# Kernel optimization log

Hardware: AMD Instinct MI355X
Metric: run time of the kernel (lower is better)

## Reference

```python
import jax, jax.numpy as jnp
import numpy as np

N_NODES = 50000
N_EDGES = 600000
D = 128
R = 8


def setup_inputs() -> dict:
    key = jax.random.key(0)
    ks = jax.random.split(key, 10)
    return {
        "node_ids": jnp.arange(N_NODES, dtype=jnp.int32),
        "src": jax.random.randint(ks[0], (N_EDGES,), 0, N_NODES, dtype=jnp.int32),
        "dst": jax.random.randint(ks[1], (N_EDGES,), 0, N_NODES, dtype=jnp.int32),
        "etype": jax.random.randint(ks[2], (N_EDGES,), 0, R, dtype=jnp.int32),
        "emb": jax.random.normal(ks[3], (N_NODES, D), dtype=jnp.float32) * 0.02,
        "W1": jax.random.normal(ks[4], (R, D, D), dtype=jnp.float32) * 0.05,
        "Wself1": jax.random.normal(ks[5], (D, D), dtype=jnp.float32) * 0.05,
        "b1": jnp.zeros((D,), dtype=jnp.float32),
        "W2": jax.random.normal(ks[6], (R, D, D), dtype=jnp.float32) * 0.05,
        "Wself2": jax.random.normal(ks[7], (D, D), dtype=jnp.float32) * 0.05,
        "b2": jnp.zeros((D,), dtype=jnp.float32),
    }


def rgcn_layer(h, W, Wself, b, src, dst, etype, n_nodes):
    # relation-wise transform of all node features: [R, N, d_out]
    hr = jnp.einsum('nd,rdo->rno', h, W)
    # per-edge gather of (relation, src) -> message, then scatter-sum to dst
    msgs = hr[etype, src]                                   # [E, d_out]
    agg = jax.ops.segment_sum(msgs, dst, num_segments=n_nodes)
    # self-loop + bias (activation=None, feat_drop=0)
    return agg + h @ Wself + b


def reference(node_ids, src, dst, etype, emb, W1, Wself1, b1, W2, Wself2, b2):
    h0 = emb[node_ids]                                      # embedding lookup over all nodes
    h1 = rgcn_layer(h0, W1, Wself1, b1, src, dst, etype, emb.shape[0])
    h2 = rgcn_layer(h1, W2, Wself2, b2, src, dst, etype, emb.shape[0])
    return h2
```

## Files before the change

kernel.cpp:

```cpp
#include <hip/hip_runtime.h>
#include <hip/hip_bf16.h>

#define NN 50000
#define NE 600000
#define DD 128
#define NR 8
#define NCHUNK ((NN + 255) / 256)

typedef __attribute__((ext_vector_type(8))) short bf16x8;
typedef __attribute__((ext_vector_type(4))) float f32x4;

__device__ __forceinline__ unsigned short f2bf(float f) {
  __hip_bfloat16 h = __float2bfloat16(f);
  return *reinterpret_cast<unsigned short*>(&h);
}
__device__ __forceinline__ unsigned pk2(float lo, float hi) {
  return (unsigned)f2bf(lo) | ((unsigned)f2bf(hi) << 16);
}
__device__ __forceinline__ float bflo(unsigned u) { return __uint_as_float(u << 16); }
__device__ __forceinline__ float bfhi(unsigned u) { return __uint_as_float(u & 0xffff0000u); }

__global__ __launch_bounds__(128) void convw_kernel(
    const float* __restrict__ W1, const float* __restrict__ Ws1,
    const float* __restrict__ W2, const float* __restrict__ Ws2,
    unsigned short* __restrict__ WT)
{
  const int m = blockIdx.y, o = blockIdx.x, d = threadIdx.x;
  const float* src;
  if (m < 8)       src = W1 + (size_t)m * DD * DD;
  else if (m == 8) src = Ws1;
  else if (m < 17) src = W2 + (size_t)(m - 9) * DD * DD;
  else             src = Ws2;
  WT[(size_t)m * DD * DD + o * DD + d] = f2bf(src[(size_t)d * DD + o]);
}

template<int AF32, int OUTF32>
__global__ __launch_bounds__(256) void transform_mfma(
    const void* __restrict__ hin, const int* __restrict__ ids,
    const unsigned short* __restrict__ WT,
    const float* __restrict__ bias,
    unsigned short* __restrict__ hr,
    void* __restrict__ outSelf)
{
  __shared__ __align__(16) char ldsW[2][DD * DD * 2];

  const int tid = threadIdx.x;
  const int rowBase = blockIdx.x * 128;
  const int lane = tid & 63;
  const int w = tid >> 6;
  const int c = lane & 15;
  const int g = lane >> 4;
  int nn[2], nld[2];
#pragma unroll
  for (int u = 0; u < 2; ++u) {
    nn[u] = rowBase + w * 32 + u * 16 + c;
    nld[u] = (nn[u] < NN) ? nn[u] : (NN - 1);
  }

  bf16x8 hfrag[2][4];
#pragma unroll
  for (int u = 0; u < 2; ++u) {
    if (AF32) {
      const int srcRow = ids[nld[u]];
      const float* hrow = (const float*)hin + (size_t)srcRow * DD;
#pragma unroll
      for (int ks = 0; ks < 4; ++ks) {
        const float4 x = *reinterpret_cast<const float4*>(hrow + ks * 32 + g * 8);
        const float4 y = *reinterpret_cast<const float4*>(hrow + ks * 32 + g * 8 + 4);
        uint4 q;
        q.x = pk2(x.x, x.y); q.y = pk2(x.z, x.w);
        q.z = pk2(y.x, y.y); q.w = pk2(y.z, y.w);
        hfrag[u][ks] = *reinterpret_cast<bf16x8*>(&q);
      }
    } else {
      const unsigned short* hrow = (const unsigned short*)hin + (size_t)nld[u] * DD;
#pragma unroll
      for (int ks = 0; ks < 4; ++ks) {
        uint4 q = *reinterpret_cast<const uint4*>(hrow + ks * 32 + g * 8);
        hfrag[u][ks] = *reinterpret_cast<bf16x8*>(&q);
      }
    }
  }

  int srcOff[8];
#pragma unroll
  for (int j = 0; j < 8; ++j) {
    const int dstB = (tid + j * 256) * 16;
    const int srcB = dstB ^ (((dstB >> 8) & 7) << 4);
    srcOff[j] = srcB >> 1;
  }

  uint4 wreg[8];
#pragma unroll
  for (int j = 0; j < 8; ++j)
    wreg[j] = *reinterpret_cast<const uint4*>(WT + srcOff[j]);
#pragma unroll
  for (int j = 0; j < 8; ++j)
    *reinterpret_cast<uint4*>(ldsW[0] + (tid + j * 256) * 16) = wreg[j];

  for (int r = 0; r < NR + 1; ++r) {
    __syncthreads();
    const char* buf = ldsW[r & 1];

    if (r < NR) {
      const unsigned short* wnext = WT + (size_t)(r + 1) * DD * DD;
#pragma unroll
      for (int j = 0; j < 8; ++j)
        wreg[j] = *reinterpret_cast<const uint4*>(wnext + srcOff[j]);
    }

    f32x4 acc[2][8];
#pragma unroll
    for (int u = 0; u < 2; ++u)
#pragma unroll
      for (int t = 0; t < 8; ++t) acc[u][t] = (f32x4){0.f, 0.f, 0.f, 0.f};
#pragma unroll
    for (int ks = 0; ks < 4; ++ks) {
#pragma unroll
      for (int t = 0; t < 8; ++t) {
        const int addr = (((t * 16 + c) << 8) + (ks << 6) + (g << 4)) ^ ((c & 7) << 4);
        bf16x8 a = *reinterpret_cast<const bf16x8*>(buf + addr);
        acc[0][t] = __builtin_amdgcn_mfma_f32_16x16x32_bf16(a, hfrag[0][ks], acc[0][t], 0, 0, 0);
        acc[1][t] = __builtin_amdgcn_mfma_f32_16x16x32_bf16(a, hfrag[1][ks], acc[1][t], 0, 0, 0);
      }
    }

#pragma unroll
    for (int u = 0; u < 2; ++u) {
      const int n = nn[u];
      if (n >= NN) continue;
      if (r < NR) {
        unsigned short* dst = hr + ((size_t)r * NN + n) * DD;
#pragma unroll
        for (int t = 0; t < 8; ++t) {
          const int o0 = t * 16 + g * 4;
          uint2 q;
          q.x = pk2(acc[u][t][0], acc[u][t][1]);
          q.y = pk2(acc[u][t][2], acc[u][t][3]);
          *reinterpret_cast<uint2*>(dst + o0) = q;
        }
      } else if (OUTF32) {
        float* dst = (float*)outSelf + (size_t)n * DD;
#pragma unroll
        for (int t = 0; t < 8; ++t) {
          const int o0 = t * 16 + g * 4;
          const float4 bv = *reinterpret_cast<const float4*>(bias + o0);
          float4 o;
          o.x = acc[u][t][0] + bv.x; o.y = acc[u][t][1] + bv.y;
          o.z = acc[u][t][2] + bv.z; o.w = acc[u][t][3] + bv.w;
          *reinterpret_cast<float4*>(dst + o0) = o;
        }
      } else {
        unsigned short* dst = (unsigned short*)outSelf + (size_t)n * DD;
#pragma unroll
        for (int t = 0; t < 8; ++t) {
          const int o0 = t * 16 + g * 4;
          const float4 bv = *reinterpret_cast<const float4*>(bias + o0);
          uint2 q;
          q.x = pk2(acc[u][t][0] + bv.x, acc[u][t][1] + bv.y);
          q.y = pk2(acc[u][t][2] + bv.z, acc[u][t][3] + bv.w);
          *reinterpret_cast<uint2*>(dst + o0) = q;
        }
      }
    }

    if (r < NR) {
      char* nbuf = ldsW[(r & 1) ^ 1];
#pragma unroll
      for (int j = 0; j < 8; ++j)
        *reinterpret_cast<uint4*>(nbuf + (tid + j * 256) * 16) = wreg[j];
    }
  }
}

__global__ __launch_bounds__(256) void hist_kernel(
    const int* __restrict__ dst, int* __restrict__ deg)
{
  const int e = blockIdx.x * 256 + threadIdx.x;
  if (e < NE) atomicAdd(&deg[dst[e]], 1);
}

__global__ __launch_bounds__(256) void bsum_kernel(
    const int* __restrict__ deg, int* __restrict__ bsum)
{
  __shared__ int tmp[256];
  const int t = threadIdx.x;
  const int i = blockIdx.x * 256 + t;
  tmp[t] = (i < NN) ? deg[i] : 0;
  __syncthreads();
#pragma unroll
  for (int off = 128; off > 0; off >>= 1) {
    if (t < off) tmp[t] += tmp[t + off];
    __syncthreads();
  }
  if (t == 0) bsum[blockIdx.x] = tmp[0];
}

__global__ __launch_bounds__(256) void bscan_kernel(
    const int* __restrict__ bsum, int* __restrict__ bbase)
{
  __shared__ int tmp[256];
  const int t = threadIdx.x;
  const int v = (t < NCHUNK) ? bsum[t] : 0;
  tmp[t] = v;
  __syncthreads();
#pragma unroll
  for (int off = 1; off < 256; off <<= 1) {
    const int x = (t >= off) ? tmp[t - off] : 0;
    __syncthreads();
    tmp[t] += x;
    __syncthreads();
  }
  if (t < NCHUNK) bbase[t] = tmp[t] - v;
}

__global__ __launch_bounds__(256) void expand_kernel(
    int* deg, const int* __restrict__ bbase, int* __restrict__ offsets)
{
  __shared__ int tmp[256];
  const int t = threadIdx.x;
  const int i = blockIdx.x * 256 + t;
  const int v = (i < NN) ? deg[i] : 0;
  tmp[t] = v;
  __syncthreads();
#pragma unroll
  for (int off = 1; off < 256; off <<= 1) {
    const int x = (t >= off) ? tmp[t - off] : 0;
    __syncthreads();
    tmp[t] += x;
    __syncthreads();
  }
  const int base = bbase[blockIdx.x];
  const int excl = base + tmp[t] - v;
  if (i < NN) {
    offsets[i] = excl;
    deg[i] = excl;
    if (i == NN - 1) offsets[NN] = base + tmp[t];
  }
}

__global__ __launch_bounds__(256) void fill_kernel(
    const int* __restrict__ src, const int* __restrict__ dst,
    const int* __restrict__ et, int* __restrict__ cursor,
    int* __restrict__ eidx)
{
  const int e = blockIdx.x * 256 + threadIdx.x;
  if (e < NE) {
    const int pos = atomicAdd(&cursor[dst[e]], 1);
    eidx[pos] = et[e] * NN + src[e];
  }
}

template<int BF16OUT>
__global__ __launch_bounds__(256) void aggregate_kernel(
    const unsigned short* __restrict__ hr,
    const int* __restrict__ offsets, const int* __restrict__ eidx,
    void* __restrict__ outv)
{
  const int node = blockIdx.x * 4 + (threadIdx.x >> 6);
  const int lane = threadIdx.x & 63;
  if (node >= NN) return;
  const int beg = offsets[node];
  const int end = offsets[node + 1];

  float a0 = 0.f, a1 = 0.f;
  int e = beg;
  for (; e + 3 < end; e += 4) {
    const int r0 = eidx[e], r1 = eidx[e + 1], r2 = eidx[e + 2], r3 = eidx[e + 3];
    const unsigned u0 = *reinterpret_cast<const unsigned*>(hr + (size_t)r0 * DD + lane * 2);
    const unsigned u1 = *reinterpret_cast<const unsigned*>(hr + (size_t)r1 * DD + lane * 2);
    const unsigned u2 = *reinterpret_cast<const unsigned*>(hr + (size_t)r2 * DD + lane * 2);
    const unsigned u3 = *reinterpret_cast<const unsigned*>(hr + (size_t)r3 * DD + lane * 2);
    a0 += (bflo(u0) + bflo(u1)) + (bflo(u2) + bflo(u3));
    a1 += (bfhi(u0) + bfhi(u1)) + (bfhi(u2) + bfhi(u3));
  }
  for (; e < end; ++e) {
    const unsigned u0 = *reinterpret_cast<const unsigned*>(hr + (size_t)eidx[e] * DD + lane * 2);
    a0 += bflo(u0);
    a1 += bfhi(u0);
  }

  if (BF16OUT) {
    unsigned* o = reinterpret_cast<unsigned*>((unsigned short*)outv + (size_t)node * DD + lane * 2);
    const unsigned u = *o;
    *o = pk2(bflo(u) + a0, bfhi(u) + a1);
  } else {
    float2* o = reinterpret_cast<float2*>((float*)outv + (size_t)node * DD + lane * 2);
    float2 v = *o;
    v.x += a0; v.y += a1;
    *o = v;
  }
}

extern "C" void kernel_launch(void* const* d_in, const int* in_sizes, int n_in,
                              void* d_out, int out_size, void* d_ws, size_t ws_size,
                              hipStream_t stream) {
  const int*   node_ids = (const int*)d_in[0];
  const int*   src   = (const int*)d_in[1];
  const int*   dst   = (const int*)d_in[2];
  const int*   etype = (const int*)d_in[3];
  const float* emb   = (const float*)d_in[4];
  const float* W1    = (const float*)d_in[5];
  const float* Ws1   = (const float*)d_in[6];
  const float* b1    = (const float*)d_in[7];
  const float* W2    = (const float*)d_in[8];
  const float* Ws2   = (const float*)d_in[9];
  const float* b2    = (const float*)d_in[10];

  char* p = (char*)d_ws;
  unsigned short* hr   = (unsigned short*)p;  p += (size_t)NR * NN * DD * 2;
  unsigned short* h1bf = (unsigned short*)p;  p += (size_t)NN * DD * 2;
  unsigned short* WT   = (unsigned short*)p;  p += (size_t)18 * DD * DD * 2;
  int* offsets         = (int*)p;             p += (size_t)(NN + 1) * 4;
  int* deg             = (int*)p;             p += (size_t)NN * 4;
  int* eidx            = (int*)p;             p += (size_t)NE * 4;
  int* bsum            = (int*)p;             p += 256 * 4;
  int* bbase           = (int*)p;

  const int eb = (NE + 255) / 256;
  const int tb = (NN + 127) / 128;
  const int ab = (NN + 3) / 4;

  convw_kernel<<<dim3(DD, 18), 128, 0, stream>>>(W1, Ws1, W2, Ws2, WT);
  hipMemsetAsync(deg, 0, (size_t)NN * 4, stream);
  hist_kernel<<<eb, 256, 0, stream>>>(dst, deg);
  bsum_kernel<<<NCHUNK, 256, 0, stream>>>(deg, bsum);
  bscan_kernel<<<1, 256, 0, stream>>>(bsum, bbase);
  expand_kernel<<<NCHUNK, 256, 0, stream>>>(deg, bbase, offsets);
  fill_kernel<<<eb, 256, 0, stream>>>(src, dst, etype, deg, eidx);

  transform_mfma<1, 0><<<tb, 256, 0, stream>>>(emb, node_ids, WT, b1, hr, h1bf);
  aggregate_kernel<1><<<ab, 256, 0, stream>>>(hr, offsets, eidx, h1bf);
  transform_mfma<0, 1><<<tb, 256, 0, stream>>>(h1bf, nullptr, WT + (size_t)9 * DD * DD, b2, hr, (float*)d_out);
  aggregate_kernel<0><<<ab, 256, 0, stream>>>(hr, offsets, eidx, (float*)d_out);
}
```

Before: 253.4 us.

## Aggregate per-relation neighbor features first, then apply one concatenated GEMM

```diff
diff --git a/kernel.cpp b/kernel.cpp
--- a/kernel.cpp
+++ b/kernel.cpp
@@ -34,13 +34,155 @@
   WT[(size_t)m * DD * DD + o * DD + d] = f2bf(src[(size_t)d * DD + o]);
 }
 
-template<int AF32, int OUTF32>
-__global__ __launch_bounds__(256) void transform_mfma(
-    const void* __restrict__ hin, const int* __restrict__ ids,
-    const unsigned short* __restrict__ WT,
+__global__ __launch_bounds__(256) void convh_kernel(
+    const float* __restrict__ emb, const int* __restrict__ ids,
+    unsigned short* __restrict__ h)
+{
+  const int gid = blockIdx.x * 256 + threadIdx.x;
+  if (gid >= NN * 16) return;
+  const int row = gid >> 4;
+  const int off = (gid & 15) * 8;
+  const int srcRow = ids[row];
+  const float* src = emb + (size_t)srcRow * DD + off;
+  const float4 a = *reinterpret_cast<const float4*>(src);
+  const float4 b = *reinterpret_cast<const float4*>(src + 4);
+  uint4 u;
+  u.x = pk2(a.x, a.y); u.y = pk2(a.z, a.w);
+  u.z = pk2(b.x, b.y); u.w = pk2(b.z, b.w);
+  *reinterpret_cast<uint4*>(h + (size_t)row * DD + off) = u;
+}
+
+__global__ __launch_bounds__(256) void hist_kernel(
+    const int* __restrict__ dst, int* __restrict__ deg)
+{
+  const int e = blockIdx.x * 256 + threadIdx.x;
+  if (e < NE) atomicAdd(&deg[dst[e]], 1);
+}
+
+__global__ __launch_bounds__(256) void bsum_kernel(
+    const int* __restrict__ deg, int* __restrict__ bsum)
+{
+  __shared__ int tmp[256];
+  const int t = threadIdx.x;
+  const int i = blockIdx.x * 256 + t;
+  tmp[t] = (i < NN) ? deg[i] : 0;
+  __syncthreads();
+#pragma unroll
+  for (int off = 128; off > 0; off >>= 1) {
+    if (t < off) tmp[t] += tmp[t + off];
+    __syncthreads();
+  }
+  if (t == 0) bsum[blockIdx.x] = tmp[0];
+}
+
+__global__ __launch_bounds__(256) void bscan_kernel(
+    const int* __restrict__ bsum, int* __restrict__ bbase)
+{
+  __shared__ int tmp[256];
+  const int t = threadIdx.x;
+  const int v = (t < NCHUNK) ? bsum[t] : 0;
+  tmp[t] = v;
+  __syncthreads();
+#pragma unroll
+  for (int off = 1; off < 256; off <<= 1) {
+    const int x = (t >= off) ? tmp[t - off] : 0;
+    __syncthreads();
+    tmp[t] += x;
+    __syncthreads();
+  }
+  if (t < NCHUNK) bbase[t] = tmp[t] - v;
+}
+
+__global__ __launch_bounds__(256) void expand_kernel(
+    int* deg, const int* __restrict__ bbase, int* __restrict__ offsets)
+{
+  __shared__ int tmp[256];
+  const int t = threadIdx.x;
+  const int i = blockIdx.x * 256 + t;
+  const int v = (i < NN) ? deg[i] : 0;
+  tmp[t] = v;
+  __syncthreads();
+#pragma unroll
+  for (int off = 1; off < 256; off <<= 1) {
+    const int x = (t >= off) ? tmp[t - off] : 0;
+    __syncthreads();
+    tmp[t] += x;
+    __syncthreads();
+  }
+  const int base = bbase[blockIdx.x];
+  const int excl = base + tmp[t] - v;
+  if (i < NN) {
+    offsets[i] = excl;
+    deg[i] = excl;
+    if (i == NN - 1) offsets[NN] = base + tmp[t];
+  }
+}
+
+__global__ __launch_bounds__(256) void fill_kernel(
+    const int* __restrict__ src, const int* __restrict__ dst,
+    const int* __restrict__ et, int* __restrict__ cursor,
+    int* __restrict__ eidx)
+{
+  const int e = blockIdx.x * 256 + threadIdx.x;
+  if (e < NE) {
+    const int pos = atomicAdd(&cursor[dst[e]], 1);
+    eidx[pos] = (src[e] << 3) | et[e];
+  }
+}
+
+__global__ __launch_bounds__(256) void agg_kernel(
+    const unsigned short* __restrict__ h,
+    const int* __restrict__ offsets, const int* __restrict__ eidx,
+    unsigned short* __restrict__ s)
+{
+  const int node = blockIdx.x * 4 + (threadIdx.x >> 6);
+  const int lane = threadIdx.x & 63;
+  if (node >= NN) return;
+  const int beg = offsets[node];
+  const int end = offsets[node + 1];
+
+  float ax[NR], ay[NR];
+#pragma unroll
+  for (int r = 0; r < NR; ++r) { ax[r] = 0.f; ay[r] = 0.f; }
+
+  int e = beg;
+  for (; e + 1 < end; e += 2) {
+    const int v0 = eidx[e], v1 = eidx[e + 1];
+    const unsigned u0 = *reinterpret_cast<const unsigned*>(h + (size_t)(v0 >> 3) * DD + lane * 2);
+    const unsigned u1 = *reinterpret_cast<const unsigned*>(h + (size_t)(v1 >> 3) * DD + lane * 2);
+    const int e0 = v0 & 7, e1 = v1 & 7;
+    const float x0 = bflo(u0), y0 = bfhi(u0), x1 = bflo(u1), y1 = bfhi(u1);
+#pragma unroll
+    for (int r = 0; r < NR; ++r) {
+      ax[r] += ((e0 == r) ? x0 : 0.f) + ((e1 == r) ? x1 : 0.f);
+      ay[r] += ((e0 == r) ? y0 : 0.f) + ((e1 == r) ? y1 : 0.f);
+    }
+  }
+  if (e < end) {
+    const int v0 = eidx[e];
+    const unsigned u0 = *reinterpret_cast<const unsigned*>(h + (size_t)(v0 >> 3) * DD + lane * 2);
+    const int e0 = v0 & 7;
+    const float x0 = bflo(u0), y0 = bfhi(u0);
+#pragma unroll
+    for (int r = 0; r < NR; ++r) {
+      ax[r] += (e0 == r) ? x0 : 0.f;
+      ay[r] += (e0 == r) ? y0 : 0.f;
+    }
+  }
+
+  unsigned short* srow = s + (size_t)node * (NR * DD) + lane * 2;
+#pragma unroll
+  for (int r = 0; r < NR; ++r)
+    *reinterpret_cast<unsigned*>(srow + r * DD) = pk2(ax[r], ay[r]);
+}
+
+template<int OUTF32>
+__global__ __launch_bounds__(256) void gemm_kernel(
+    const unsigned short* __restrict__ hbuf,
+    const unsigned short* __restrict__ s,
+    const unsigned short* __restrict__ WTl,
     const float* __restrict__ bias,
-    unsigned short* __restrict__ hr,
-    void* __restrict__ outSelf)
+    void* __restrict__ out)
 {
   __shared__ __align__(16) char ldsW[2][DD * DD * 2];
 
@@ -57,31 +199,6 @@
     nld[u] = (nn[u] < NN) ? nn[u] : (NN - 1);
   }
 
-  bf16x8 hfrag[2][4];
-#pragma unroll
-  for (int u = 0; u < 2; ++u) {
-    if (AF32) {
-      const int srcRow = ids[nld[u]];
-      const float* hrow = (const float*)hin + (size_t)srcRow * DD;
-#pragma unroll
-      for (int ks = 0; ks < 4; ++ks) {
-        const float4 x = *reinterpret_cast<const float4*>(hrow + ks * 32 + g * 8);
-        const float4 y = *reinterpret_cast<const float4*>(hrow + ks * 32 + g * 8 + 4);
-        uint4 q;
-        q.x = pk2(x.x, x.y); q.y = pk2(x.z, x.w);
-        q.z = pk2(y.x, y.y); q.w = pk2(y.z, y.w);
-        hfrag[u][ks] = *reinterpret_cast<bf16x8*>(&q);
-      }
-    } else {
-      const unsigned short* hrow = (const unsigned short*)hin + (size_t)nld[u] * DD;
-#pragma unroll
-      for (int ks = 0; ks < 4; ++ks) {
-        uint4 q = *reinterpret_cast<const uint4*>(hrow + ks * 32 + g * 8);
-        hfrag[u][ks] = *reinterpret_cast<bf16x8*>(&q);
-      }
-    }
-  }
-
   int srcOff[8];
 #pragma unroll
   for (int j = 0; j < 8; ++j) {
@@ -93,202 +210,95 @@
   uint4 wreg[8];
 #pragma unroll
   for (int j = 0; j < 8; ++j)
-    wreg[j] = *reinterpret_cast<const uint4*>(WT + srcOff[j]);
+    wreg[j] = *reinterpret_cast<const uint4*>(WTl + srcOff[j]);
 #pragma unroll
   for (int j = 0; j < 8; ++j)
     *reinterpret_cast<uint4*>(ldsW[0] + (tid + j * 256) * 16) = wreg[j];
 
-  for (int r = 0; r < NR + 1; ++r) {
-    __syncthreads();
-    const char* buf = ldsW[r & 1];
-
-    if (r < NR) {
-      const unsigned short* wnext = WT + (size_t)(r + 1) * DD * DD;
-#pragma unroll
-      for (int j = 0; j < 8; ++j)
-        wreg[j] = *reinterpret_cast<const uint4*>(wnext + srcOff[j]);
-    }
-
-    f32x4 acc[2][8];
-#pragma unroll
-    for (int u = 0; u < 2; ++u)
-#pragma unroll
-      for (int t = 0; t < 8; ++t) acc[u][t] = (f32x4){0.f, 0.f, 0.f, 0.f};
-#pragma unroll
-    for (int ks = 0; ks < 4; ++ks) {
+  bf16x8 sfA[2][4], sfB[2][4];
+#pragma unroll
+  for (int u = 0; u < 2; ++u) {
+    const unsigned short* p0 = s + (size_t)nld[u] * (NR * DD);
+#pragma unroll
+    for (int ks = 0; ks < 4; ++ks)
+      sfA[u][ks] = *reinterpret_cast<const bf16x8*>(p0 + ks * 32 + g * 8);
+  }
+
+  f32x4 acc[2][8];
+#pragma unroll
+  for (int u = 0; u < 2; ++u)
+#pragma unroll
+    for (int t = 0; t < 8; ++t) acc[u][t] = (f32x4){0.f, 0.f, 0.f, 0.f};
+
+#define GSTEP(R, CUR, NXT)                                                            \
+  {                                                                                   \
+    __syncthreads();                                                                  \
+    const char* buf = ldsW[(R) & 1];                                                  \
+    if ((R) < NR) {                                                                   \
+      const unsigned short* wnext = WTl + (size_t)((R) + 1) * DD * DD;                \
+      _Pragma("unroll")                                                               \
+      for (int j = 0; j < 8; ++j)                                                     \
+        wreg[j] = *reinterpret_cast<const uint4*>(wnext + srcOff[j]);                 \
+      _Pragma("unroll")                                                               \
+      for (int u = 0; u < 2; ++u) {                                                   \
+        const unsigned short* pn = ((R) + 1 < NR)                                     \
+            ? s + (size_t)nld[u] * (NR * DD) + ((R) + 1) * DD                         \
+            : hbuf + (size_t)nld[u] * DD;                                             \
+        _Pragma("unroll")                                                             \
+        for (int ks = 0; ks < 4; ++ks)                                                \
+          NXT[u][ks] = *reinterpret_cast<const bf16x8*>(pn + ks * 32 + g * 8);        \
+      }                                                                               \
+    }                                                                                 \
+    _Pragma("unroll")                                                                 \
+    for (int ks = 0; ks < 4; ++ks) {                                                  \
+      _Pragma("unroll")                                                               \
+      for (int t = 0; t < 8; ++t) {                                                   \
+        const int addr = (((t * 16 + c) << 8) + (ks << 6) + (g << 4)) ^ ((c & 7) << 4); \
+        bf16x8 a = *reinterpret_cast<const bf16x8*>(buf + addr);                      \
+        acc[0][t] = __builtin_amdgcn_mfma_f32_16x16x32_bf16(a, CUR[0][ks], acc[0][t], 0, 0, 0); \
+        acc[1][t] = __builtin_amdgcn_mfma_f32_16x16x32_bf16(a, CUR[1][ks], acc[1][t], 0, 0, 0); \
+      }                                                                               \
+    }                                                                                 \
+    if ((R) < NR) {                                                                   \
+      char* nbuf = ldsW[((R) & 1) ^ 1];                                               \
+      _Pragma("unroll")                                                               \
+      for (int j = 0; j < 8; ++j)                                                     \
+        *reinterpret_cast<uint4*>(nbuf + (tid + j * 256) * 16) = wreg[j];             \
+    }                                                                                 \
+  }
+
+  GSTEP(0, sfA, sfB) GSTEP(1, sfB, sfA) GSTEP(2, sfA, sfB) GSTEP(3, sfB, sfA)
+  GSTEP(4, sfA, sfB) GSTEP(5, sfB, sfA) GSTEP(6, sfA, sfB) GSTEP(7, sfB, sfA)
+  GSTEP(8, sfA, sfB)
+#undef GSTEP
+
+#pragma unroll
+  for (int u = 0; u < 2; ++u) {
+    const int n = nn[u];
+    if (n >= NN) continue;
+    if (OUTF32) {
+      float* dst = (float*)out + (size_t)n * DD;
 #pragma unroll
       for (int t = 0; t < 8; ++t) {
-        const int addr = (((t * 16 + c) << 8) + (ks << 6) + (g << 4)) ^ ((c & 7) << 4);
-        bf16x8 a = *reinterpret_cast<const bf16x8*>(buf + addr);
-        acc[0][t] = __builtin_amdgcn_mfma_f32_16x16x32_bf16(a, hfrag[0][ks], acc[0][t], 0, 0, 0);
-        acc[1][t] = __builtin_amdgcn_mfma_f32_16x16x32_bf16(a, hfrag[1][ks], acc[1][t], 0, 0, 0);
+        const int o0 = t * 16 + g * 4;
+        const float4 bv = *reinterpret_cast<const float4*>(bias + o0);
+        float4 o;
+        o.x = acc[u][t][0] + bv.x; o.y = acc[u][t][1] + bv.y;
+        o.z = acc[u][t][2] + bv.z; o.w = acc[u][t][3] + bv.w;
+        *reinterpret_cast<float4*>(dst + o0) = o;
+      }
+    } else {
+      unsigned short* dst = (unsigned short*)out + (size_t)n * DD;
+#pragma unroll
+      for (int t = 0; t < 8; ++t) {
+        const int o0 = t * 16 + g * 4;
+        const float4 bv = *reinterpret_cast<const float4*>(bias + o0);
+        uint2 q;
+        q.x = pk2(acc[u][t][0] + bv.x, acc[u][t][1] + bv.y);
+        q.y = pk2(acc[u][t][2] + bv.z, acc[u][t][3] + bv.w);
+        *reinterpret_cast<uint2*>(dst + o0) = q;
       }
     }
-
-#pragma unroll
-    for (int u = 0; u < 2; ++u) {
-      const int n = nn[u];
-      if (n >= NN) continue;
-      if (r < NR) {
-        unsigned short* dst = hr + ((size_t)r * NN + n) * DD;
-#pragma unroll
-        for (int t = 0; t < 8; ++t) {
-          const int o0 = t * 16 + g * 4;
-          uint2 q;
-          q.x = pk2(acc[u][t][0], acc[u][t][1]);
-          q.y = pk2(acc[u][t][2], acc[u][t][3]);
-          *reinterpret_cast<uint2*>(dst + o0) = q;
-        }
-      } else if (OUTF32) {
-        float* dst = (float*)outSelf + (size_t)n * DD;
-#pragma unroll
-        for (int t = 0; t < 8; ++t) {
-          const int o0 = t * 16 + g * 4;
-          const float4 bv = *reinterpret_cast<const float4*>(bias + o0);
-          float4 o;
-          o.x = acc[u][t][0] + bv.x; o.y = acc[u][t][1] + bv.y;
-          o.z = acc[u][t][2] + bv.z; o.w = acc[u][t][3] + bv.w;
-          *reinterpret_cast<float4*>(dst + o0) = o;
-        }
-      } else {
-        unsigned short* dst = (unsigned short*)outSelf + (size_t)n * DD;
-#pragma unroll
-        for (int t = 0; t < 8; ++t) {
-          const int o0 = t * 16 + g * 4;
-          const float4 bv = *reinterpret_cast<const float4*>(bias + o0);
-          uint2 q;
-          q.x = pk2(acc[u][t][0] + bv.x, acc[u][t][1] + bv.y);
-          q.y = pk2(acc[u][t][2] + bv.z, acc[u][t][3] + bv.w);
-          *reinterpret_cast<uint2*>(dst + o0) = q;
-        }
-      }
-    }
-
-    if (r < NR) {
-      char* nbuf = ldsW[(r & 1) ^ 1];
-#pragma unroll
-      for (int j = 0; j < 8; ++j)
-        *reinterpret_cast<uint4*>(nbuf + (tid + j * 256) * 16) = wreg[j];
-    }
-  }
-}
-
-__global__ __launch_bounds__(256) void hist_kernel(
-    const int* __restrict__ dst, int* __restrict__ deg)
-{
-  const int e = blockIdx.x * 256 + threadIdx.x;
-  if (e < NE) atomicAdd(&deg[dst[e]], 1);
-}
-
-__global__ __launch_bounds__(256) void bsum_kernel(
-    const int* __restrict__ deg, int* __restrict__ bsum)
-{
-  __shared__ int tmp[256];
-  const int t = threadIdx.x;
-  const int i = blockIdx.x * 256 + t;
-  tmp[t] = (i < NN) ? deg[i] : 0;
-  __syncthreads();
-#pragma unroll
-  for (int off = 128; off > 0; off >>= 1) {
-    if (t < off) tmp[t] += tmp[t + off];
-    __syncthreads();
-  }
-  if (t == 0) bsum[blockIdx.x] = tmp[0];
-}
-
-__global__ __launch_bounds__(256) void bscan_kernel(
-    const int* __restrict__ bsum, int* __restrict__ bbase)
-{
-  __shared__ int tmp[256];
-  const int t = threadIdx.x;
-  const int v = (t < NCHUNK) ? bsum[t] : 0;
-  tmp[t] = v;
-  __syncthreads();
-#pragma unroll
-  for (int off = 1; off < 256; off <<= 1) {
-    const int x = (t >= off) ? tmp[t - off] : 0;
-    __syncthreads();
-    tmp[t] += x;
-    __syncthreads();
-  }
-  if (t < NCHUNK) bbase[t] = tmp[t] - v;
-}
-
-__global__ __launch_bounds__(256) void expand_kernel(
-    int* deg, const int* __restrict__ bbase, int* __restrict__ offsets)
-{
-  __shared__ int tmp[256];
-  const int t = threadIdx.x;
-  const int i = blockIdx.x * 256 + t;
-  const int v = (i < NN) ? deg[i] : 0;
-  tmp[t] = v;
-  __syncthreads();
-#pragma unroll
-  for (int off = 1; off < 256; off <<= 1) {
-    const int x = (t >= off) ? tmp[t - off] : 0;
-    __syncthreads();
-    tmp[t] += x;
-    __syncthreads();
-  }
-  const int base = bbase[blockIdx.x];
-  const int excl = base + tmp[t] - v;
-  if (i < NN) {
-    offsets[i] = excl;
-    deg[i] = excl;
-    if (i == NN - 1) offsets[NN] = base + tmp[t];
-  }
-}
-
-__global__ __launch_bounds__(256) void fill_kernel(
-    const int* __restrict__ src, const int* __restrict__ dst,
-    const int* __restrict__ et, int* __restrict__ cursor,
-    int* __restrict__ eidx)
-{
-  const int e = blockIdx.x * 256 + threadIdx.x;
-  if (e < NE) {
-    const int pos = atomicAdd(&cursor[dst[e]], 1);
-    eidx[pos] = et[e] * NN + src[e];
-  }
-}
-
-template<int BF16OUT>
-__global__ __launch_bounds__(256) void aggregate_kernel(
-    const unsigned short* __restrict__ hr,
-    const int* __restrict__ offsets, const int* __restrict__ eidx,
-    void* __restrict__ outv)
-{
-  const int node = blockIdx.x * 4 + (threadIdx.x >> 6);
-  const int lane = threadIdx.x & 63;
-  if (node >= NN) return;
-  const int beg = offsets[node];
-  const int end = offsets[node + 1];
-
-  float a0 = 0.f, a1 = 0.f;
-  int e = beg;
-  for (; e + 3 < end; e += 4) {
-    const int r0 = eidx[e], r1 = eidx[e + 1], r2 = eidx[e + 2], r3 = eidx[e + 3];
-    const unsigned u0 = *reinterpret_cast<const unsigned*>(hr + (size_t)r0 * DD + lane * 2);
-    const unsigned u1 = *reinterpret_cast<const unsigned*>(hr + (size_t)r1 * DD + lane * 2);
-    const unsigned u2 = *reinterpret_cast<const unsigned*>(hr + (size_t)r2 * DD + lane * 2);
-    const unsigned u3 = *reinterpret_cast<const unsigned*>(hr + (size_t)r3 * DD + lane * 2);
-    a0 += (bflo(u0) + bflo(u1)) + (bflo(u2) + bflo(u3));
-    a1 += (bfhi(u0) + bfhi(u1)) + (bfhi(u2) + bfhi(u3));
-  }
-  for (; e < end; ++e) {
-    const unsigned u0 = *reinterpret_cast<const unsigned*>(hr + (size_t)eidx[e] * DD + lane * 2);
-    a0 += bflo(u0);
-    a1 += bfhi(u0);
-  }
-
-  if (BF16OUT) {
-    unsigned* o = reinterpret_cast<unsigned*>((unsigned short*)outv + (size_t)node * DD + lane * 2);
-    const unsigned u = *o;
-    *o = pk2(bflo(u) + a0, bfhi(u) + a1);
-  } else {
-    float2* o = reinterpret_cast<float2*>((float*)outv + (size_t)node * DD + lane * 2);
-    float2 v = *o;
-    v.x += a0; v.y += a1;
-    *o = v;
   }
 }
 
@@ -308,8 +318,8 @@
   const float* b2    = (const float*)d_in[10];
 
   char* p = (char*)d_ws;
-  unsigned short* hr   = (unsigned short*)p;  p += (size_t)NR * NN * DD * 2;
-  unsigned short* h1bf = (unsigned short*)p;  p += (size_t)NN * DD * 2;
+  unsigned short* s    = (unsigned short*)p;  p += (size_t)NN * NR * DD * 2;
+  unsigned short* hbuf = (unsigned short*)p;  p += (size_t)NN * DD * 2;
   unsigned short* WT   = (unsigned short*)p;  p += (size_t)18 * DD * DD * 2;
   int* offsets         = (int*)p;             p += (size_t)(NN + 1) * 4;
   int* deg             = (int*)p;             p += (size_t)NN * 4;
@@ -322,6 +332,7 @@
   const int ab = (NN + 3) / 4;
 
   convw_kernel<<<dim3(DD, 18), 128, 0, stream>>>(W1, Ws1, W2, Ws2, WT);
+  convh_kernel<<<(NN * 16) / 256, 256, 0, stream>>>(emb, node_ids, hbuf);
   hipMemsetAsync(deg, 0, (size_t)NN * 4, stream);
   hist_kernel<<<eb, 256, 0, stream>>>(dst, deg);
   bsum_kernel<<<NCHUNK, 256, 0, stream>>>(deg, bsum);
@@ -329,8 +340,8 @@
   expand_kernel<<<NCHUNK, 256, 0, stream>>>(deg, bbase, offsets);
   fill_kernel<<<eb, 256, 0, stream>>>(src, dst, etype, deg, eidx);
 
-  transform_mfma<1, 0><<<tb, 256, 0, stream>>>(emb, node_ids, WT, b1, hr, h1bf);
-  aggregate_kernel<1><<<ab, 256, 0, stream>>>(hr, offsets, eidx, h1bf);
-  transform_mfma<0, 1><<<tb, 256, 0, stream>>>(h1bf, nullptr, WT + (size_t)9 * DD * DD, b2, hr, (float*)d_out);
-  aggregate_kernel<0><<<ab, 256, 0, stream>>>(hr, offsets, eidx, (float*)d_out);
-}
+  agg_kernel<<<ab, 256, 0, stream>>>(hbuf, offsets, eidx, s);
+  gemm_kernel<0><<<tb, 256, 0, stream>>>(hbuf, s, WT, b1, hbuf);
+  agg_kernel<<<ab, 256, 0, stream>>>(hbuf, offsets, eidx, s);
+  gemm_kernel<1><<<tb, 256, 0, stream>>>(hbuf, s, WT + (size_t)9 * DD * DD, b2, (float*)d_out);
+}
```

Result: slower. 259.4 us (+2.4%).
